# Kernel optimization log

Hardware: AMD Instinct MI355X
Metric: run time of the kernel (lower is better)

## Reference

```python
import jax, jax.numpy as jnp
import numpy as np

NT, NA, NB, E, D = 100000, 50000, 50000, 500000, 128
BN_EPS = 1e-5


def _mlp2(h, W1, b1, g, beta, W2, b2):
    # Linear -> BatchNorm1d (training-mode batch stats) -> ReLU -> Linear
    z = h @ W1 + b1
    mu = jnp.mean(z, axis=0, keepdims=True)
    var = jnp.mean((z - mu) ** 2, axis=0, keepdims=True)  # biased var, as torch BN
    z = jax.nn.relu((z - mu) * jax.lax.rsqrt(var + BN_EPS) * g + beta)
    return z @ W2 + b2


def setup_inputs() -> dict:
    key = jax.random.key(0)
    ks = jax.random.split(key, 24)
    s = 1.0 / np.sqrt(D)

    def lin(k):
        kw, kb = jax.random.split(k)
        return (jax.random.uniform(kw, (D, D), jnp.float32, -s, s),
                jax.random.uniform(kb, (D,), jnp.float32, -s, s))

    inp = {
        "hT": jax.random.normal(ks[0], (NT, D), jnp.float32),
        "hA": jax.random.normal(ks[1], (NA, D), jnp.float32),
        "hB": jax.random.normal(ks[2], (NB, D), jnp.float32),
        "src_ta": jax.random.randint(ks[3], (E,), 0, NT),
        "dst_ta": jax.random.randint(ks[4], (E,), 0, NA),
        "src_tb": jax.random.randint(ks[5], (E,), 0, NT),
        "dst_tb": jax.random.randint(ks[6], (E,), 0, NB),
        "src_at": jax.random.randint(ks[7], (E,), 0, NA),
        "dst_at": jax.random.randint(ks[8], (E,), 0, NT),
        "src_bt": jax.random.randint(ks[9], (E,), 0, NB),
        "dst_bt": jax.random.randint(ks[10], (E,), 0, NT),
        "eps_ta": jnp.zeros((1,), jnp.float32),
        "eps_tb": jnp.zeros((1,), jnp.float32),
        "eps_ret": jnp.zeros((1,), jnp.float32),
    }
    for i, n in enumerate(["ta", "tb", "ret"]):
        W1, b1 = lin(ks[11 + 2 * i])
        W2, b2 = lin(ks[12 + 2 * i])
        inp[n + "_W1"], inp[n + "_b1"] = W1, b1
        inp[n + "_g"] = jnp.ones((D,), jnp.float32)
        inp[n + "_beta"] = jnp.zeros((D,), jnp.float32)
        inp[n + "_W2"], inp[n + "_b2"] = W2, b2
    inp["Wp"], inp["bp"] = lin(ks[20])
    return inp


def reference(hT, hA, hB, src_ta, dst_ta, src_tb, dst_tb, src_at, dst_at,
              src_bt, dst_bt, eps_ta, eps_tb, eps_ret,
              ta_W1, ta_b1, ta_g, ta_beta, ta_W2, ta_b2,
              tb_W1, tb_b1, tb_g, tb_beta, tb_W2, tb_b2,
              ret_W1, ret_b1, ret_g, ret_beta, ret_W2, ret_b2, Wp, bp):
    # go paths: copy_src('h','m') + sum -> 'a' on neighbor types, then GIN MLP
    aA = jax.ops.segment_sum(hT[src_ta], dst_ta, num_segments=NA)   # [NA, D]
    hA_new = _mlp2((1.0 + eps_ta) * hA + aA, ta_W1, ta_b1, ta_g, ta_beta, ta_W2, ta_b2)
    aB = jax.ops.segment_sum(hT[src_tb], dst_tb, num_segments=NB)   # [NB, D]
    hB_new = _mlp2((1.0 + eps_tb) * hB + aB, tb_W1, tb_b1, tb_g, tb_beta, tb_W2, tb_b2)
    # return paths: multi_send_and_recv with 'sum' cross-etype reducer
    aT = (jax.ops.segment_sum(hA_new[src_at], dst_at, num_segments=NT)
          + jax.ops.segment_sum(hB_new[src_bt], dst_bt, num_segments=NT))  # [NT, D]
    hT_proj = hT @ Wp + bp
    hT_new = _mlp2((1.0 + eps_ret) * hT_proj + aT,
                   ret_W1, ret_b1, ret_g, ret_beta, ret_W2, ret_b2)
    return (hT_new, hA_new, hB_new)
```

## Files before the change

### kernel.cpp

```cpp
#include <hip/hip_runtime.h>

#define NTT 100000
#define NAA 50000
#define NBB 50000
#define NEE 500000
#define DD  128
#define NPART 64
#define MLP_GRID 2048

typedef short s16x8 __attribute__((ext_vector_type(8)));
typedef float f32x4 __attribute__((ext_vector_type(4)));
typedef unsigned short ushort_t;

__device__ inline float bf2f(unsigned short u) {
    union { unsigned int i; float f; } c;
    c.i = ((unsigned int)u) << 16;
    return c.f;
}

struct WP { const float* p[7]; };

__global__ __launch_bounds__(256) void wconv_kernel(WP wp, ushort_t* out) {
    int idx = blockIdx.x * 256 + threadIdx.x;
    if (idx >= 7 * 16384) return;
    int m = idx >> 14;
    int r = idx & 16383;
    int col = r >> 7;
    int k = r & 127;
    float v = wp.p[m][k * 128 + col];
    union { __bf16 b; unsigned short u; } cv;
    cv.b = (__bf16)v;
    out[idx] = cv.u;
}

__global__ __launch_bounds__(256) void scatter_pk_kernel(const float* __restrict__ feat,
                                                         const int* __restrict__ src,
                                                         const int* __restrict__ dst,
                                                         ushort_t* agg, int nE) {
    int gtid = blockIdx.x * blockDim.x + threadIdx.x;
    int wid = gtid >> 6;
    int l = gtid & 63;
    int nw = (gridDim.x * blockDim.x) >> 6;
    for (int e = wid; e < nE; e += nw) {
        int s = src[e];
        int d = dst[e];
        const float2 v = *(const float2*)(feat + (size_t)s * DD + 2 * l);
        union { __bf16 b[2]; unsigned int u; } p;
        p.b[0] = (__bf16)v.x;
        p.b[1] = (__bf16)v.y;
        ushort_t* pa = agg + (size_t)d * DD + 2 * l;
        asm volatile("global_atomic_pk_add_bf16 %0, %1, off"
                     :: "v"(pa), "v"(p.u) : "memory");
    }
}

template <int MODE>
__global__ __launch_bounds__(256) void mlp_kernel(const void* __restrict__ Xv,
                                                  const void* __restrict__ Av,
                                                  const float* __restrict__ eps_ptr,
                                                  const float* __restrict__ ss,
                                                  const ushort_t* __restrict__ Wt,
                                                  const float* __restrict__ bias,
                                                  void* __restrict__ outv,
                                                  float* __restrict__ statsp,
                                                  int ntiles) {
    const float* X = (const float*)Xv;
    const ushort_t* Xb = (const ushort_t*)Xv;
    const ushort_t* A = (const ushort_t*)Av;
    float* out = (float*)outv;
    ushort_t* outb = (ushort_t*)outv;

    const int tid = threadIdx.x;
    const int w = tid >> 6;
    const int l = tid & 63;
    const int rl = l & 15;
    const int grp = l >> 4;
    const int wcol = w * 32;

    s16x8 bq[2][4];
#pragma unroll
    for (int ct = 0; ct < 2; ++ct)
#pragma unroll
        for (int kc = 0; kc < 4; ++kc)
            bq[ct][kc] = *(const s16x8*)(Wt + (size_t)(wcol + ct * 16 + rl) * DD + kc * 32 + grp * 8);

    const float eps1 = (MODE == 0 || MODE == 3) ? (1.f + eps_ptr[0]) : 0.f;
    float bias_c[2];
#pragma unroll
    for (int ct = 0; ct < 2; ++ct) bias_c[ct] = bias[wcol + ct * 16 + rl];

    float st_s[2] = {0.f, 0.f}, st_q[2] = {0.f, 0.f};

    for (int t = blockIdx.x; t < ntiles; t += gridDim.x) {
        const size_t xbase = (size_t)(t * 16 + rl) * DD;
        s16x8 af[4];
#pragma unroll
        for (int kc = 0; kc < 4; ++kc) {
            const int k0 = kc * 32 + grp * 8;
            if (MODE == 1) {
                af[kc] = *(const s16x8*)(Xb + xbase + k0);
            } else {
                float4 v0 = *(const float4*)(X + xbase + k0);
                float4 v1 = *(const float4*)(X + xbase + k0 + 4);
                if (MODE == 0) {
                    s16x8 av = *(const s16x8*)(A + xbase + k0);
                    v0.x = eps1 * v0.x + bf2f((unsigned short)av[0]);
                    v0.y = eps1 * v0.y + bf2f((unsigned short)av[1]);
                    v0.z = eps1 * v0.z + bf2f((unsigned short)av[2]);
                    v0.w = eps1 * v0.w + bf2f((unsigned short)av[3]);
                    v1.x = eps1 * v1.x + bf2f((unsigned short)av[4]);
                    v1.y = eps1 * v1.y + bf2f((unsigned short)av[5]);
                    v1.z = eps1 * v1.z + bf2f((unsigned short)av[6]);
                    v1.w = eps1 * v1.w + bf2f((unsigned short)av[7]);
                } else if (MODE == 2) {
                    float4 c0 = *(const float4*)(ss + k0);
                    float4 c1 = *(const float4*)(ss + k0 + 4);
                    float4 s0 = *(const float4*)(ss + 128 + k0);
                    float4 s1 = *(const float4*)(ss + 128 + k0 + 4);
                    v0.x = fmaxf(v0.x * c0.x + s0.x, 0.f); v0.y = fmaxf(v0.y * c0.y + s0.y, 0.f);
                    v0.z = fmaxf(v0.z * c0.z + s0.z, 0.f); v0.w = fmaxf(v0.w * c0.w + s0.w, 0.f);
                    v1.x = fmaxf(v1.x * c1.x + s1.x, 0.f); v1.y = fmaxf(v1.y * c1.y + s1.y, 0.f);
                    v1.z = fmaxf(v1.z * c1.z + s1.z, 0.f); v1.w = fmaxf(v1.w * c1.w + s1.w, 0.f);
                }
                union { __bf16 h[8]; s16x8 v; } u;
                u.h[0] = (__bf16)v0.x; u.h[1] = (__bf16)v0.y;
                u.h[2] = (__bf16)v0.z; u.h[3] = (__bf16)v0.w;
                u.h[4] = (__bf16)v1.x; u.h[5] = (__bf16)v1.y;
                u.h[6] = (__bf16)v1.z; u.h[7] = (__bf16)v1.w;
                af[kc] = u.v;
            }
        }

        if (MODE == 2) __syncthreads();

        f32x4 acc[2] = {{0.f, 0.f, 0.f, 0.f}, {0.f, 0.f, 0.f, 0.f}};
#pragma unroll
        for (int kc = 0; kc < 4; ++kc) {
            acc[0] = __builtin_amdgcn_mfma_f32_16x16x32_bf16(af[kc], bq[0][kc], acc[0], 0, 0, 0);
            acc[1] = __builtin_amdgcn_mfma_f32_16x16x32_bf16(af[kc], bq[1][kc], acc[1], 0, 0, 0);
        }

#pragma unroll
        for (int ct = 0; ct < 2; ++ct) {
            const int col = wcol + ct * 16 + rl;
#pragma unroll
            for (int r = 0; r < 4; ++r) {
                const int row = t * 16 + grp * 4 + r;
                float zv = acc[ct][r] + bias_c[ct];
                if (MODE == 3) {
                    ushort_t* po = outb + (size_t)row * DD + col;
                    zv = eps1 * zv + bf2f(*po);
                    union { __bf16 b; unsigned short u; } cv;
                    cv.b = (__bf16)zv;
                    *po = cv.u;
                } else {
                    out[(size_t)row * DD + col] = zv;
                }
                if (MODE == 0 || MODE == 1) {
                    st_s[ct] += zv;
                    st_q[ct] += zv * zv;
                }
            }
        }
    }

    if (MODE == 0 || MODE == 1) {
        const int part = blockIdx.x & (NPART - 1);
#pragma unroll
        for (int ct = 0; ct < 2; ++ct) {
            st_s[ct] += __shfl_xor(st_s[ct], 16);
            st_s[ct] += __shfl_xor(st_s[ct], 32);
            st_q[ct] += __shfl_xor(st_q[ct], 16);
            st_q[ct] += __shfl_xor(st_q[ct], 32);
            if (grp == 0) {
                const int col = wcol + ct * 16 + rl;
                unsafeAtomicAdd(&statsp[part * 256 + col], st_s[ct]);
                unsafeAtomicAdd(&statsp[part * 256 + 128 + col], st_q[ct]);
            }
        }
    }
}

__global__ void bnfin_kernel(const float* __restrict__ statsp,
                             const float* __restrict__ g,
                             const float* __restrict__ beta,
                             float invN, float* ss) {
    int c = threadIdx.x;
    float s = 0.f, q = 0.f;
    for (int p = 0; p < NPART; ++p) {
        s += statsp[p * 256 + c];
        q += statsp[p * 256 + 128 + c];
    }
    float mu = s * invN;
    float var = q * invN - mu * mu;
    float sc = g[c] * rsqrtf(var + 1e-5f);
    ss[c] = sc;
    ss[128 + c] = beta[c] - mu * sc;
}


extern "C" void kernel_launch(void* const* d_in, const int* in_sizes, int n_in,
                              void* d_out, int out_size, void* d_ws, size_t ws_size,
                              hipStream_t stream) {
    const float* hT = (const float*)d_in[0];
    const float* hA = (const float*)d_in[1];
    const float* hB = (const float*)d_in[2];
    const int* src_ta = (const int*)d_in[3];
    const int* dst_ta = (const int*)d_in[4];
    const int* src_tb = (const int*)d_in[5];
    const int* dst_tb = (const int*)d_in[6];
    const int* src_at = (const int*)d_in[7];
    const int* dst_at = (const int*)d_in[8];
    const int* src_bt = (const int*)d_in[9];
    const int* dst_bt = (const int*)d_in[10];
    const float* eps_ta = (const float*)d_in[11];
    const float* eps_tb = (const float*)d_in[12];
    const float* eps_ret = (const float*)d_in[13];
    const float* ta_b1 = (const float*)d_in[15];
    const float* ta_g = (const float*)d_in[16];
    const float* ta_beta = (const float*)d_in[17];
    const float* ta_b2 = (const float*)d_in[19];
    const float* tb_b1 = (const float*)d_in[21];
    const float* tb_g = (const float*)d_in[22];
    const float* tb_beta = (const float*)d_in[23];
    const float* tb_b2 = (const float*)d_in[25];
    const float* ret_b1 = (const float*)d_in[27];
    const float* ret_g = (const float*)d_in[28];
    const float* ret_beta = (const float*)d_in[29];
    const float* ret_b2 = (const float*)d_in[31];
    const float* bp = (const float*)d_in[33];

    float* out = (float*)d_out;
    float* zT  = out;
    float* hAn = out + (size_t)NTT * DD;
    float* hBn = hAn + (size_t)NAA * DD;
    float* zA = zT;
    float* zB = zT + (size_t)NAA * DD;

    char* ws = (char*)d_ws;
    ushort_t* aggA = (ushort_t*)ws;
    ushort_t* aggB = aggA + (size_t)NAA * DD;
    ushort_t* aggT = aggB + (size_t)NBB * DD;
    ushort_t* Wt   = aggT + (size_t)NTT * DD;
    float* statsp = (float*)(Wt + 7 * 16384);
    float* ssb = statsp + 3 * NPART * 256;

    hipMemsetAsync(aggA, 0, (size_t)(NAA + NBB + NTT) * DD * 2, stream);
    hipMemsetAsync(statsp, 0, (size_t)3 * NPART * 256 * 4, stream);

    WP wp;
    wp.p[0] = (const float*)d_in[14];
    wp.p[1] = (const float*)d_in[18];
    wp.p[2] = (const float*)d_in[20];
    wp.p[3] = (const float*)d_in[24];
    wp.p[4] = (const float*)d_in[26];
    wp.p[5] = (const float*)d_in[30];
    wp.p[6] = (const float*)d_in[32];
    wconv_kernel<<<(7 * 16384 + 255) / 256, 256, 0, stream>>>(wp, Wt);

    scatter_pk_kernel<<<2048, 256, 0, stream>>>(hT, src_ta, dst_ta, aggA, NEE);
    scatter_pk_kernel<<<2048, 256, 0, stream>>>(hT, src_tb, dst_tb, aggB, NEE);

    mlp_kernel<0><<<MLP_GRID, 256, 0, stream>>>(hA, aggA, eps_ta, nullptr,
                                                Wt + 0 * 16384, ta_b1, zA,
                                                statsp + 0 * NPART * 256, NAA / 16);
    bnfin_kernel<<<1, 128, 0, stream>>>(statsp + 0 * NPART * 256, ta_g, ta_beta,
                                        1.f / NAA, ssb + 0);
    mlp_kernel<2><<<MLP_GRID, 256, 0, stream>>>(zA, nullptr, nullptr, ssb + 0,
                                                Wt + 1 * 16384, ta_b2, hAn,
                                                nullptr, NAA / 16);

    mlp_kernel<0><<<MLP_GRID, 256, 0, stream>>>(hB, aggB, eps_tb, nullptr,
                                                Wt + 2 * 16384, tb_b1, zB,
                                                statsp + 1 * NPART * 256, NBB / 16);
    bnfin_kernel<<<1, 128, 0, stream>>>(statsp + 1 * NPART * 256, tb_g, tb_beta,
                                        1.f / NBB, ssb + 256);
    mlp_kernel<2><<<MLP_GRID, 256, 0, stream>>>(zB, nullptr, nullptr, ssb + 256,
                                                Wt + 3 * 16384, tb_b2, hBn,
                                                nullptr, NBB / 16);

    scatter_pk_kernel<<<2048, 256, 0, stream>>>(hAn, src_at, dst_at, aggT, NEE);
    scatter_pk_kernel<<<2048, 256, 0, stream>>>(hBn, src_bt, dst_bt, aggT, NEE);

    mlp_kernel<3><<<MLP_GRID, 256, 0, stream>>>(hT, nullptr, eps_ret, nullptr,
                                                Wt + 6 * 16384, bp, aggT,
                                                nullptr, NTT / 16);

    mlp_kernel<1><<<MLP_GRID, 256, 0, stream>>>(aggT, nullptr, nullptr, nullptr,
                                                Wt + 4 * 16384, ret_b1, zT,
                                                statsp + 2 * NPART * 256, NTT / 16);
    bnfin_kernel<<<1, 128, 0, stream>>>(statsp + 2 * NPART * 256, ret_g, ret_beta,
                                        1.f / NTT, ssb + 512);
    mlp_kernel<2><<<MLP_GRID, 256, 0, stream>>>(zT, nullptr, nullptr, ssb + 512,
                                                Wt + 5 * 16384, ret_b2, zT,
                                                nullptr, NTT / 16);
}
```

Before: 864.0 us.

## Fuse projection with first ret linear and store intermediates as bf16

Merges the hT projection, the aggT residual add and the first ret-MLP linear into one kernel that passes each tile's intermediate through LDS, instead of a read-modify-write pass followed by a separate GEMM. Intermediate pre-BN activations zA, zB and zT are now kept as bf16 in workspace rather than fp32 in the output buffer, which roughly halves their traffic. Workspace regions are reused, so aggT gets its own memset, and the two go-path first-layer kernels are reordered. The fused kernel adds a per-tile __syncthreads, and storing z in bf16 may add some rounding error.

```diff
diff --git a/kernel.cpp b/kernel.cpp
--- a/kernel.cpp
+++ b/kernel.cpp
@@ -17,6 +17,11 @@
     c.i = ((unsigned int)u) << 16;
     return c.f;
 }
+__device__ inline ushort_t f2bf(float f) {
+    union { __bf16 b; unsigned short u; } c;
+    c.b = (__bf16)f;
+    return c.u;
+}
 
 struct WP { const float* p[7]; };
 
@@ -27,10 +32,7 @@
     int r = idx & 16383;
     int col = r >> 7;
     int k = r & 127;
-    float v = wp.p[m][k * 128 + col];
-    union { __bf16 b; unsigned short u; } cv;
-    cv.b = (__bf16)v;
-    out[idx] = cv.u;
+    out[idx] = f2bf(wp.p[m][k * 128 + col]);
 }
 
 __global__ __launch_bounds__(256) void scatter_pk_kernel(const float* __restrict__ feat,
@@ -56,7 +58,7 @@
 
 template <int MODE>
 __global__ __launch_bounds__(256) void mlp_kernel(const void* __restrict__ Xv,
-                                                  const void* __restrict__ Av,
+                                                  const ushort_t* __restrict__ A,
                                                   const float* __restrict__ eps_ptr,
                                                   const float* __restrict__ ss,
                                                   const ushort_t* __restrict__ Wt,
@@ -66,7 +68,6 @@
                                                   int ntiles) {
     const float* X = (const float*)Xv;
     const ushort_t* Xb = (const ushort_t*)Xv;
-    const ushort_t* A = (const ushort_t*)Av;
     float* out = (float*)outv;
     ushort_t* outb = (ushort_t*)outv;
 
@@ -84,7 +85,7 @@
         for (int kc = 0; kc < 4; ++kc)
             bq[ct][kc] = *(const s16x8*)(Wt + (size_t)(wcol + ct * 16 + rl) * DD + kc * 32 + grp * 8);
 
-    const float eps1 = (MODE == 0 || MODE == 3) ? (1.f + eps_ptr[0]) : 0.f;
+    const float eps1 = (MODE == 0) ? (1.f + eps_ptr[0]) : 0.f;
     float bias_c[2];
 #pragma unroll
     for (int ct = 0; ct < 2; ++ct) bias_c[ct] = bias[wcol + ct * 16 + rl];
@@ -97,41 +98,38 @@
 #pragma unroll
         for (int kc = 0; kc < 4; ++kc) {
             const int k0 = kc * 32 + grp * 8;
-            if (MODE == 1) {
-                af[kc] = *(const s16x8*)(Xb + xbase + k0);
-            } else {
+            if (MODE == 0) {
                 float4 v0 = *(const float4*)(X + xbase + k0);
                 float4 v1 = *(const float4*)(X + xbase + k0 + 4);
-                if (MODE == 0) {
-                    s16x8 av = *(const s16x8*)(A + xbase + k0);
-                    v0.x = eps1 * v0.x + bf2f((unsigned short)av[0]);
-                    v0.y = eps1 * v0.y + bf2f((unsigned short)av[1]);
-                    v0.z = eps1 * v0.z + bf2f((unsigned short)av[2]);
-                    v0.w = eps1 * v0.w + bf2f((unsigned short)av[3]);
-                    v1.x = eps1 * v1.x + bf2f((unsigned short)av[4]);
-                    v1.y = eps1 * v1.y + bf2f((unsigned short)av[5]);
-                    v1.z = eps1 * v1.z + bf2f((unsigned short)av[6]);
-                    v1.w = eps1 * v1.w + bf2f((unsigned short)av[7]);
-                } else if (MODE == 2) {
-                    float4 c0 = *(const float4*)(ss + k0);
-                    float4 c1 = *(const float4*)(ss + k0 + 4);
-                    float4 s0 = *(const float4*)(ss + 128 + k0);
-                    float4 s1 = *(const float4*)(ss + 128 + k0 + 4);
-                    v0.x = fmaxf(v0.x * c0.x + s0.x, 0.f); v0.y = fmaxf(v0.y * c0.y + s0.y, 0.f);
-                    v0.z = fmaxf(v0.z * c0.z + s0.z, 0.f); v0.w = fmaxf(v0.w * c0.w + s0.w, 0.f);
-                    v1.x = fmaxf(v1.x * c1.x + s1.x, 0.f); v1.y = fmaxf(v1.y * c1.y + s1.y, 0.f);
-                    v1.z = fmaxf(v1.z * c1.z + s1.z, 0.f); v1.w = fmaxf(v1.w * c1.w + s1.w, 0.f);
-                }
+                s16x8 av = *(const s16x8*)(A + xbase + k0);
                 union { __bf16 h[8]; s16x8 v; } u;
-                u.h[0] = (__bf16)v0.x; u.h[1] = (__bf16)v0.y;
-                u.h[2] = (__bf16)v0.z; u.h[3] = (__bf16)v0.w;
-                u.h[4] = (__bf16)v1.x; u.h[5] = (__bf16)v1.y;
-                u.h[6] = (__bf16)v1.z; u.h[7] = (__bf16)v1.w;
+                u.h[0] = (__bf16)(eps1 * v0.x + bf2f((unsigned short)av[0]));
+                u.h[1] = (__bf16)(eps1 * v0.y + bf2f((unsigned short)av[1]));
+                u.h[2] = (__bf16)(eps1 * v0.z + bf2f((unsigned short)av[2]));
+                u.h[3] = (__bf16)(eps1 * v0.w + bf2f((unsigned short)av[3]));
+                u.h[4] = (__bf16)(eps1 * v1.x + bf2f((unsigned short)av[4]));
+                u.h[5] = (__bf16)(eps1 * v1.y + bf2f((unsigned short)av[5]));
+                u.h[6] = (__bf16)(eps1 * v1.z + bf2f((unsigned short)av[6]));
+                u.h[7] = (__bf16)(eps1 * v1.w + bf2f((unsigned short)av[7]));
+                af[kc] = u.v;
+            } else {
+                s16x8 xv = *(const s16x8*)(Xb + xbase + k0);
+                float4 c0 = *(const float4*)(ss + k0);
+                float4 c1 = *(const float4*)(ss + k0 + 4);
+                float4 s0 = *(const float4*)(ss + 128 + k0);
+                float4 s1 = *(const float4*)(ss + 128 + k0 + 4);
+                union { __bf16 h[8]; s16x8 v; } u;
+                u.h[0] = (__bf16)fmaxf(bf2f((unsigned short)xv[0]) * c0.x + s0.x, 0.f);
+                u.h[1] = (__bf16)fmaxf(bf2f((unsigned short)xv[1]) * c0.y + s0.y, 0.f);
+                u.h[2] = (__bf16)fmaxf(bf2f((unsigned short)xv[2]) * c0.z + s0.z, 0.f);
+                u.h[3] = (__bf16)fmaxf(bf2f((unsigned short)xv[3]) * c0.w + s0.w, 0.f);
+                u.h[4] = (__bf16)fmaxf(bf2f((unsigned short)xv[4]) * c1.x + s1.x, 0.f);
+                u.h[5] = (__bf16)fmaxf(bf2f((unsigned short)xv[5]) * c1.y + s1.y, 0.f);
+                u.h[6] = (__bf16)fmaxf(bf2f((unsigned short)xv[6]) * c1.z + s1.z, 0.f);
+                u.h[7] = (__bf16)fmaxf(bf2f((unsigned short)xv[7]) * c1.w + s1.w, 0.f);
                 af[kc] = u.v;
             }
         }
-
-        if (MODE == 2) __syncthreads();
 
         f32x4 acc[2] = {{0.f, 0.f, 0.f, 0.f}, {0.f, 0.f, 0.f, 0.f}};
 #pragma unroll
@@ -147,24 +145,18 @@
             for (int r = 0; r < 4; ++r) {
                 const int row = t * 16 + grp * 4 + r;
                 float zv = acc[ct][r] + bias_c[ct];
-                if (MODE == 3) {
-                    ushort_t* po = outb + (size_t)row * DD + col;
-                    zv = eps1 * zv + bf2f(*po);
-                    union { __bf16 b; unsigned short u; } cv;
-                    cv.b = (__bf16)zv;
-                    *po = cv.u;
+                if (MODE == 0) {
+                    outb[(size_t)row * DD + col] = f2bf(zv);
+                    st_s[ct] += zv;
+                    st_q[ct] += zv * zv;
                 } else {
                     out[(size_t)row * DD + col] = zv;
                 }
-                if (MODE == 0 || MODE == 1) {
-                    st_s[ct] += zv;
-                    st_q[ct] += zv * zv;
-                }
             }
         }
     }
 
-    if (MODE == 0 || MODE == 1) {
+    if (MODE == 0) {
         const int part = blockIdx.x & (NPART - 1);
 #pragma unroll
         for (int ct = 0; ct < 2; ++ct) {
@@ -177,6 +169,123 @@
                 unsafeAtomicAdd(&statsp[part * 256 + col], st_s[ct]);
                 unsafeAtomicAdd(&statsp[part * 256 + 128 + col], st_q[ct]);
             }
+        }
+    }
+}
+
+__global__ __launch_bounds__(256) void mode4_kernel(const float* __restrict__ hT,
+                                                    const ushort_t* __restrict__ aggT,
+                                                    const float* __restrict__ eps_ptr,
+                                                    const ushort_t* __restrict__ Wpt,
+                                                    const float* __restrict__ bp,
+                                                    const ushort_t* __restrict__ W1t,
+                                                    const float* __restrict__ b1,
+                                                    ushort_t* __restrict__ zb,
+                                                    float* __restrict__ statsp,
+                                                    int ntiles) {
+    __shared__ __align__(16) ushort_t u_lds[2][16][136];
+    const int tid = threadIdx.x;
+    const int w = tid >> 6;
+    const int l = tid & 63;
+    const int rl = l & 15;
+    const int grp = l >> 4;
+    const int wcol = w * 32;
+
+    s16x8 bqp[2][4], bqr[2][4];
+#pragma unroll
+    for (int ct = 0; ct < 2; ++ct)
+#pragma unroll
+        for (int kc = 0; kc < 4; ++kc) {
+            const size_t off = (size_t)(wcol + ct * 16 + rl) * DD + kc * 32 + grp * 8;
+            bqp[ct][kc] = *(const s16x8*)(Wpt + off);
+            bqr[ct][kc] = *(const s16x8*)(W1t + off);
+        }
+
+    const float eps1 = 1.f + eps_ptr[0];
+    float bpc[2], b1c[2];
+#pragma unroll
+    for (int ct = 0; ct < 2; ++ct) {
+        bpc[ct] = bp[wcol + ct * 16 + rl];
+        b1c[ct] = b1[wcol + ct * 16 + rl];
+    }
+
+    float st_s[2] = {0.f, 0.f}, st_q[2] = {0.f, 0.f};
+    int buf = 0;
+
+    for (int t = blockIdx.x; t < ntiles; t += gridDim.x) {
+        const size_t xbase = (size_t)(t * 16 + rl) * DD;
+        s16x8 af[4];
+#pragma unroll
+        for (int kc = 0; kc < 4; ++kc) {
+            const int k0 = kc * 32 + grp * 8;
+            float4 v0 = *(const float4*)(hT + xbase + k0);
+            float4 v1 = *(const float4*)(hT + xbase + k0 + 4);
+            union { __bf16 h[8]; s16x8 v; } u;
+            u.h[0] = (__bf16)v0.x; u.h[1] = (__bf16)v0.y;
+            u.h[2] = (__bf16)v0.z; u.h[3] = (__bf16)v0.w;
+            u.h[4] = (__bf16)v1.x; u.h[5] = (__bf16)v1.y;
+            u.h[6] = (__bf16)v1.z; u.h[7] = (__bf16)v1.w;
+            af[kc] = u.v;
+        }
+
+        f32x4 acc1[2] = {{0.f, 0.f, 0.f, 0.f}, {0.f, 0.f, 0.f, 0.f}};
+#pragma unroll
+        for (int kc = 0; kc < 4; ++kc) {
+            acc1[0] = __builtin_amdgcn_mfma_f32_16x16x32_bf16(af[kc], bqp[0][kc], acc1[0], 0, 0, 0);
+            acc1[1] = __builtin_amdgcn_mfma_f32_16x16x32_bf16(af[kc], bqp[1][kc], acc1[1], 0, 0, 0);
+        }
+
+#pragma unroll
+        for (int ct = 0; ct < 2; ++ct) {
+            const int col = wcol + ct * 16 + rl;
+#pragma unroll
+            for (int r = 0; r < 4; ++r) {
+                const int lrow = grp * 4 + r;
+                const size_t row = (size_t)(t * 16 + lrow);
+                float uv = eps1 * (acc1[ct][r] + bpc[ct]) + bf2f(aggT[row * DD + col]);
+                u_lds[buf][lrow][col] = f2bf(uv);
+            }
+        }
+        __syncthreads();
+
+        s16x8 af2[4];
+#pragma unroll
+        for (int kc = 0; kc < 4; ++kc)
+            af2[kc] = *(const s16x8*)&u_lds[buf][rl][kc * 32 + grp * 8];
+
+        f32x4 acc2[2] = {{0.f, 0.f, 0.f, 0.f}, {0.f, 0.f, 0.f, 0.f}};
+#pragma unroll
+        for (int kc = 0; kc < 4; ++kc) {
+            acc2[0] = __builtin_amdgcn_mfma_f32_16x16x32_bf16(af2[kc], bqr[0][kc], acc2[0], 0, 0, 0);
+            acc2[1] = __builtin_amdgcn_mfma_f32_16x16x32_bf16(af2[kc], bqr[1][kc], acc2[1], 0, 0, 0);
+        }
+
+#pragma unroll
+        for (int ct = 0; ct < 2; ++ct) {
+            const int col = wcol + ct * 16 + rl;
+#pragma unroll
+            for (int r = 0; r < 4; ++r) {
+                const int row = t * 16 + grp * 4 + r;
+                float zv = acc2[ct][r] + b1c[ct];
+                zb[(size_t)row * DD + col] = f2bf(zv);
+                st_s[ct] += zv;
+                st_q[ct] += zv * zv;
+            }
+        }
+        buf ^= 1;
+    }
+
+    const int part = blockIdx.x & (NPART - 1);
+#pragma unroll
+    for (int ct = 0; ct < 2; ++ct) {
+        st_s[ct] += __shfl_xor(st_s[ct], 16);
+        st_s[ct] += __shfl_xor(st_s[ct], 32);
+        st_q[ct] += __shfl_xor(st_q[ct], 16);
+        st_q[ct] += __shfl_xor(st_q[ct], 32);
+        if (grp == 0) {
+            const int col = wcol + ct * 16 + rl;
+            unsafeAtomicAdd(&statsp[part * 256 + col], st_s[ct]);
+            unsafeAtomicAdd(&statsp[part * 256 + 128 + col], st_q[ct]);
         }
     }
 }
@@ -231,21 +340,24 @@
     const float* bp = (const float*)d_in[33];
 
     float* out = (float*)d_out;
-    float* zT  = out;
+    float* hTn = out;
     float* hAn = out + (size_t)NTT * DD;
     float* hBn = hAn + (size_t)NAA * DD;
-    float* zA = zT;
-    float* zB = zT + (size_t)NAA * DD;
 
     char* ws = (char*)d_ws;
-    ushort_t* aggA = (ushort_t*)ws;
-    ushort_t* aggB = aggA + (size_t)NAA * DD;
-    ushort_t* aggT = aggB + (size_t)NBB * DD;
-    ushort_t* Wt   = aggT + (size_t)NTT * DD;
+    ushort_t* R0 = (ushort_t*)ws;
+    ushort_t* aggA = R0;
+    ushort_t* aggB = R0 + (size_t)NAA * DD;
+    ushort_t* zT   = R0;
+    ushort_t* R1 = R0 + (size_t)NTT * DD;
+    ushort_t* zA = R1;
+    ushort_t* zB = R1 + (size_t)NAA * DD;
+    ushort_t* aggT = R1;
+    ushort_t* Wt = R1 + (size_t)NTT * DD;
     float* statsp = (float*)(Wt + 7 * 16384);
     float* ssb = statsp + 3 * NPART * 256;
 
-    hipMemsetAsync(aggA, 0, (size_t)(NAA + NBB + NTT) * DD * 2, stream);
+    hipMemsetAsync(aggA, 0, (size_t)NTT * DD * 2, stream);
     hipMemsetAsync(statsp, 0, (size_t)3 * NPART * 256 * 4, stream);
 
     WP wp;
@@ -264,34 +376,34 @@
     mlp_kernel<0><<<MLP_GRID, 256, 0, stream>>>(hA, aggA, eps_ta, nullptr,
                                                 Wt + 0 * 16384, ta_b1, zA,
                                                 statsp + 0 * NPART * 256, NAA / 16);
+    mlp_kernel<0><<<MLP_GRID, 256, 0, stream>>>(hB, aggB, eps_tb, nullptr,
+                                                Wt + 2 * 16384, tb_b1, zB,
+                                                statsp + 1 * NPART * 256, NBB / 16);
     bnfin_kernel<<<1, 128, 0, stream>>>(statsp + 0 * NPART * 256, ta_g, ta_beta,
                                         1.f / NAA, ssb + 0);
+    bnfin_kernel<<<1, 128, 0, stream>>>(statsp + 1 * NPART * 256, tb_g, tb_beta,
+                                        1.f / NBB, ssb + 256);
+
     mlp_kernel<2><<<MLP_GRID, 256, 0, stream>>>(zA, nullptr, nullptr, ssb + 0,
                                                 Wt + 1 * 16384, ta_b2, hAn,
                                                 nullptr, NAA / 16);
-
-    mlp_kernel<0><<<MLP_GRID, 256, 0, stream>>>(hB, aggB, eps_tb, nullptr,
-                                                Wt + 2 * 16384, tb_b1, zB,
-                                                statsp + 1 * NPART * 256, NBB / 16);
-    bnfin_kernel<<<1, 128, 0, stream>>>(statsp + 1 * NPART * 256, tb_g, tb_beta,
-                                        1.f / NBB, ssb + 256);
     mlp_kernel<2><<<MLP_GRID, 256, 0, stream>>>(zB, nullptr, nullptr, ssb + 256,
                                                 Wt + 3 * 16384, tb_b2, hBn,
                                                 nullptr, NBB / 16);
 
+    hipMemsetAsync(aggT, 0, (size_t)NTT * DD * 2, stream);
+
     scatter_pk_kernel<<<2048, 256, 0, stream>>>(hAn, src_at, dst_at, aggT, NEE);
     scatter_pk_kernel<<<2048, 256, 0, stream>>>(hBn, src_bt, dst_bt, aggT, NEE);
 
-    mlp_kernel<3><<<MLP_GRID, 256, 0, stream>>>(hT, nullptr, eps_ret, nullptr,
-                                                Wt + 6 * 16384, bp, aggT,
-                                                nullptr, NTT / 16);
-
-    mlp_kernel<1><<<MLP_GRID, 256, 0, stream>>>(aggT, nullptr, nullptr, nullptr,
-                                                Wt + 4 * 16384, ret_b1, zT,
-                                                statsp + 2 * NPART * 256, NTT / 16);
+    mode4_kernel<<<MLP_GRID, 256, 0, stream>>>(hT, aggT, eps_ret,
+                                               Wt + 6 * 16384, bp,
+                                               Wt + 4 * 16384, ret_b1,
+                                               zT, statsp + 2 * NPART * 256, NTT / 16);
     bnfin_kernel<<<1, 128, 0, stream>>>(statsp + 2 * NPART * 256, ret_g, ret_beta,
                                         1.f / NTT, ssb + 512);
+
     mlp_kernel<2><<<MLP_GRID, 256, 0, stream>>>(zT, nullptr, nullptr, ssb + 512,
-                                                Wt + 5 * 16384, ret_b2, zT,
+                                                Wt + 5 * 16384, ret_b2, hTn,
                                                 nullptr, NTT / 16);
 }
```

Result: faster. 828.4 us (-4.1%).
